# Kernel tuning notes

Hardware: AMD Instinct MI355X
Metric: run time of the kernel (lower is better)

## Reference

```python
import jax, jax.numpy as jnp
import numpy as np

LEAKING_RATE = 0.5

def setup_inputs() -> dict:
    key = jax.random.key(0)
    k1, k2, k3 = jax.random.split(key, 3)
    B, T, I, R = 32, 4096, 64, 512
    x = jax.random.normal(k1, (B, T, I), dtype=jnp.float32)
    # input_projection weight ~ U(-1, 1), shape [R, I]
    w_in = jax.random.uniform(k2, (R, I), dtype=jnp.float32, minval=-1.0, maxval=1.0)
    # state_projection diagonal ~ U(-0.5, 0.5)
    d = jax.random.uniform(k3, (R,), dtype=jnp.float32, minval=-0.5, maxval=0.5)
    return {"x": x, "w_in": w_in, "d": d}

def reference(x, w_in, d):
    # Faithful to the original forward: the Python loop reads all_states[:, t, :],
    # which is ZERO at every step (never the previous state). Hence each timestep
    # is independent:
    #   state = 0
    #   new_state = tanh(d * state + x_t @ W_in^T) = tanh(x_t @ W_in^T)
    #   out_t = lr * state + (1 - lr) * new_state = (1 - lr) * tanh(x_t @ W_in^T)
    proj = jnp.einsum('bti,ri->btr', x, w_in)           # [B, T, R]
    zero_state = jnp.zeros_like(proj)
    new_state = jnp.tanh(zero_state * d + proj)
    out = LEAKING_RATE * zero_state + (1.0 - LEAKING_RATE) * new_state
    return out
```

## Files before the change

kernel.cpp:

```cpp
#include <hip/hip_runtime.h>

typedef int   i32x4 __attribute__((ext_vector_type(4)));
typedef float f32x4 __attribute__((ext_vector_type(4)));

#define M_ROWS 131072
#define N_COLS 512
#define K_DIM  64
#define MT     4
#define MAGIC  0x600DF00D

#define MFMAI8 __builtin_amdgcn_mfma_i32_16x16x64_i8

__device__ __forceinline__ int obuf_idx(int m, int r) {
  return m * 512 + (r ^ ((m & 7) << 2));
}

__device__ __forceinline__ void lds_barrier() {
  asm volatile("s_waitcnt lgkmcnt(0)" ::: "memory");
  __builtin_amdgcn_s_barrier();
  __builtin_amdgcn_sched_barrier(0);
}

__device__ __forceinline__ float half_tanh_pre(float ps) {
  float t = __builtin_amdgcn_exp2f(ps);
  return 0.5f - __builtin_amdgcn_rcpf(t + 1.0f);
}

__device__ __forceinline__ void xquant16(const float* __restrict__ p,
                                         i32x4& hi, i32x4& lo) {
#pragma unroll
  for (int c = 0; c < 4; ++c) {
    f32x4 v = *(const f32x4*)(p + 4 * c);
    int a1 = 0, a0 = 0;
#pragma unroll
    for (int j = 0; j < 4; ++j) {
      float s = __builtin_rintf(v[j] * 2048.0f);
      s = fminf(fmaxf(s, -16319.f), 16319.f);
      const int q = (int)s;
      const int h = (q + 64) >> 7;
      const int l = q - (h << 7);
      a1 |= (h & 255) << (8 * j);
      a0 |= (l & 255) << (8 * j);
    }
    hi[c] = a1; lo[c] = a0;
  }
}

__global__ void probe_k(int* __restrict__ tab,
                        i32x4* __restrict__ wq1, i32x4* __restrict__ wq0,
                        const float* __restrict__ w) {
  const int tid  = threadIdx.x;
  const int lane = tid & 63;
  const int i16  = lane & 15;
  const int g    = lane >> 4;
  const i32x4 zi = {0, 0, 0, 0};

  int pig[4];
  bool ok = true;
  {
    const int bb = (g + 1) * 0x01010101;
    const i32x4 bgv = {bb, bb, bb, bb};
#pragma unroll
    for (int g0 = 0; g0 < 4; ++g0) {
      const int ab = (g == g0) ? 0x01010101 : 0;
      const i32x4 dA = {ab, ab, ab, ab};
      i32x4 dt = MFMAI8(dA, bgv, zi, 0, 0, 0);
      const int v = dt[0] >> 4;
      bool u = (dt[0] == (v << 4)) && (v >= 1) && (v <= 4);
#pragma unroll
      for (int q = 1; q < 4; ++q) u = u && (dt[q] == dt[0]);
      ok = ok && u;
      pig[g0] = v - 1;
    }
  }
  ok = ok && (((1 << pig[0]) | (1 << pig[1]) | (1 << pig[2]) | (1 << pig[3])) == 15);
  int pinv_g = 0;
#pragma unroll
  for (int g0 = 0; g0 < 4; ++g0) if (pig[g0] == g) pinv_g = g0;

  int rowv[4], colv[4];
  {
    const int vb = i16 * 0x01010101;
    const i32x4 vals  = {vb, vb, vb, vb};
    const i32x4 onesv = {0x01010101, 0x01010101, 0x01010101, 0x01010101};
    i32x4 d1 = MFMAI8(vals, onesv, zi, 0, 0, 0);
    i32x4 d2 = MFMAI8(onesv, vals, zi, 0, 0, 0);
#pragma unroll
    for (int q = 0; q < 4; ++q) {
      rowv[q] = d1[q] >> 6;
      colv[q] = d2[q] >> 6;
      ok = ok && (d1[q] == (rowv[q] << 6)) && (rowv[q] >= 0) && (rowv[q] < 16) &&
                 (d2[q] == (colv[q] << 6)) && (colv[q] >= 0) && (colv[q] < 16);
    }
  }

  {
    i32x4 ta, tb;
#pragma unroll
    for (int c = 0; c < 4; ++c) {
      int a = 0, b = 0;
#pragma unroll
      for (int j = 0; j < 4; ++j) {
        const int ka = 16 * g + 4 * c + j;
        const int kb = 16 * pinv_g + 4 * c + j;
        const int av = ((5 * i16 + 3 * ka) & 63) - 32;
        const int bv = ((7 * kb + 11 * i16) & 63) - 32;
        a |= (av & 255) << (8 * j);
        b |= (bv & 255) << (8 * j);
      }
      ta[c] = a; tb[c] = b;
    }
    i32x4 dt3 = MFMAI8(ta, tb, zi, 0, 0, 0);
#pragma unroll
    for (int q = 0; q < 4; ++q) {
      int ref = 0;
      for (int k = 0; k < 64; ++k)
        ref += (((5 * rowv[q] + 3 * k) & 63) - 32) * (((7 * k + 11 * colv[q]) & 63) - 32);
      ok = ok && (dt3[q] == ref);
    }
  }
  const bool all_ok = __all((int)ok);
  const bool vec = all_ok &&
      __all((int)(colv[0] == colv[1] && colv[1] == colv[2] && colv[2] == colv[3] &&
                  rowv[1] == rowv[0] + 1 && rowv[2] == rowv[0] + 2 &&
                  rowv[3] == rowv[0] + 3 && (rowv[0] & 3) == 0));

  if (tid < 64) {
#pragma unroll
    for (int q = 0; q < 4; ++q) tab[lane * 4 + q] = (colv[q] << 8) | rowv[q];
    tab[256 + lane] = pinv_g;
    if (lane == 0) { tab[320] = all_ok ? MAGIC : 0; tab[321] = vec ? 1 : 0; }
  }

  if (wq1 != nullptr) {
    const float* wr = w + (size_t)tid * K_DIM;
#pragma unroll
    for (int gg = 0; gg < 4; ++gg) {
      i32x4 a1v, a0v;
#pragma unroll
      for (int c = 0; c < 4; ++c) {
        int a1 = 0, a0 = 0;
#pragma unroll
        for (int j = 0; j < 4; ++j) {
          float s = __builtin_rintf(wr[16 * gg + 4 * c + j] * 8192.0f);
          s = fminf(fmaxf(s, -8192.f), 8192.f);
          const int q = (int)s;
          const int h = (q + 64) >> 7;
          const int l = q - (h << 7);
          a1 |= (h & 255) << (8 * j);
          a0 |= (l & 255) << (8 * j);
        }
        a1v[c] = a1; a0v[c] = a0;
      }
      wq1[tid * 4 + gg] = a1v;
      wq0[tid * 4 + gg] = a0v;
    }
  }
}

__global__ __launch_bounds__(256, 4) void esn_m(const float* __restrict__ x,
                                                const float* __restrict__ w,
                                                const int* __restrict__ tab,
                                                const i32x4* __restrict__ wq1,
                                                const i32x4* __restrict__ wq0,
                                                float* __restrict__ out) {
  const int tid  = threadIdx.x;
  const int wv   = tid >> 6;
  const int lane = tid & 63;
  const int i16  = lane & 15;
  const int g    = lane >> 4;
  const int mb0  = blockIdx.x * (16 * MT);
  const i32x4 zi = {0, 0, 0, 0};

  __shared__ int   xq[MT][2][64][4];
  __shared__ float obuf[16 * 512];

  bool ok = false;
  int vecf = 0, pinv = 0;
  int rowv[4], colv[4];
  if (tab != nullptr) {
    const i32x4 rc = ((const i32x4*)tab)[lane];
#pragma unroll
    for (int q = 0; q < 4; ++q) { rowv[q] = rc[q] & 255; colv[q] = (rc[q] >> 8) & 255; }
    pinv = tab[256 + lane];
    ok   = (tab[320] == MAGIC);
    vecf = tab[321];
  }

  if (ok) {
    {
      i32x4 x1p, x0p;
      xquant16(x + (size_t)(mb0 + 16 * wv + i16) * K_DIM + 16 * pinv, x1p, x0p);
      *(i32x4*)&xq[wv][0][lane][0] = x1p;
      *(i32x4*)&xq[wv][1][lane][0] = x0p;
    }

    i32x4 w1p[8], w0p[8];
    if (wq1 != nullptr) {
#pragma unroll
      for (int t = 0; t < 8; ++t) {
        const int row = 128 * wv + 16 * t + i16;
        w1p[t] = wq1[row * 4 + g];
        w0p[t] = wq0[row * 4 + g];
      }
    } else {
#pragma unroll
      for (int t = 0; t < 8; ++t) {
        const float* wb = w + (size_t)(128 * wv + 16 * t + i16) * K_DIM + 16 * g;
#pragma unroll
        for (int c = 0; c < 4; ++c) {
          f32x4 v = *(const f32x4*)(wb + 4 * c);
          int a1 = 0, a0 = 0;
#pragma unroll
          for (int j = 0; j < 4; ++j) {
            float s = __builtin_rintf(v[j] * 8192.0f);
            s = fminf(fmaxf(s, -8192.f), 8192.f);
            const int q = (int)s;
            const int h = (q + 64) >> 7;
            const int l = q - (h << 7);
            a1 |= (h & 255) << (8 * j);
            a0 |= (l & 255) << (8 * j);
          }
          w1p[t][c] = a1; w0p[t][c] = a0;
        }
      }
    }
    __syncthreads();

    const float TANH_C = 2.8853900817779268f * 5.9604644775390625e-8f;
#pragma unroll 1
    for (int mi = 0; mi < MT; ++mi) {
      const int mb = mb0 + 16 * mi;
      const i32x4 x1p = *(const i32x4*)&xq[mi][0][lane][0];
      const i32x4 x0p = *(const i32x4*)&xq[mi][1][lane][0];

#pragma unroll
      for (int t = 0; t < 8; ++t) {
        i32x4 p11 = MFMAI8(w1p[t], x1p, zi, 0, 0, 0);
        i32x4 pm  = MFMAI8(w0p[t], x1p, zi, 0, 0, 0);
        pm        = MFMAI8(w1p[t], x0p, pm, 0, 0, 0);
        i32x4 p00 = MFMAI8(w0p[t], x0p, zi, 0, 0, 0);

        const int rb = 128 * wv + 16 * t;
        if (vecf) {
          f32x4 v;
#pragma unroll
          for (int q = 0; q < 4; ++q) {
            const float S = fmaf((float)p11[q], 16384.f,
                                 fmaf((float)pm[q], 128.f, (float)p00[q]));
            v[q] = half_tanh_pre(S * TANH_C);
          }
          *(f32x4*)&obuf[obuf_idx(colv[0], rb + rowv[0])] = v;
        } else {
#pragma unroll
          for (int q = 0; q < 4; ++q) {
            const float S = fmaf((float)p11[q], 16384.f,
                                 fmaf((float)pm[q], 128.f, (float)p00[q]));
            obuf[obuf_idx(colv[q], rb + rowv[q])] = half_tanh_pre(S * TANH_C);
          }
        }
      }
      lds_barrier();

#pragma unroll
      for (int p = 0; p < 8; ++p) {
        const int idx = p * 1024 + tid * 4;
        const int row = idx >> 9, col = idx & 511;
        const f32x4 v = *(const f32x4*)&obuf[obuf_idx(row, col)];
        *(f32x4*)(out + (size_t)mb * N_COLS + idx) = v;
      }
      if (mi + 1 < MT) lds_barrier();
    }
  } else {
#pragma unroll 1
    for (int half = 0; half < 2; ++half) {
      const int r = half * 256 + tid;
      f32x4 wr[16];
      const f32x4* wp = (const f32x4*)(w + (size_t)r * K_DIM);
#pragma unroll
      for (int i = 0; i < 16; ++i) wr[i] = wp[i];

      const f32x4* xrow = (const f32x4*)(x + (size_t)mb0 * K_DIM);
      float* orow = out + (size_t)mb0 * N_COLS + r;
#pragma unroll 1
      for (int mi = 0; mi < 16 * MT; ++mi) {
        const f32x4* xr = xrow + (size_t)mi * 16;
        f32x4 acc = {0.f, 0.f, 0.f, 0.f};
#pragma unroll
        for (int kc = 0; kc < 16; kc += 4)
#pragma unroll
          for (int j = 0; j < 4; ++j) {
            acc[0] = fmaf(xr[kc + 0][j], wr[kc + 0][j], acc[0]);
            acc[1] = fmaf(xr[kc + 1][j], wr[kc + 1][j], acc[1]);
            acc[2] = fmaf(xr[kc + 2][j], wr[kc + 2][j], acc[2]);
            acc[3] = fmaf(xr[kc + 3][j], wr[kc + 3][j], acc[3]);
          }
        const float p = (acc[0] + acc[1]) + (acc[2] + acc[3]);
        orow[(size_t)mi * N_COLS] = half_tanh_pre(p * 2.8853900817779268f);
      }
    }
  }
}

extern "C" void kernel_launch(void* const* d_in, const int* in_sizes, int n_in,
                              void* d_out, int out_size, void* d_ws, size_t ws_size,
                              hipStream_t stream) {
  const float* x = (const float*)d_in[0];
  const float* w = (const float*)d_in[1];
  float* out = (float*)d_out;

  int*   tab = (ws_size >= 2048) ? (int*)d_ws : nullptr;
  i32x4* wq1 = nullptr;
  i32x4* wq0 = nullptr;
  if (ws_size >= 4096 + 2 * 32768) {
    wq1 = (i32x4*)((char*)d_ws + 4096);
    wq0 = (i32x4*)((char*)d_ws + 4096 + 32768);
  }
  if (tab) hipLaunchKernelGGL(probe_k, dim3(1), dim3(512), 0, stream,
                              tab, wq1, wq0, w);

  dim3 grid(M_ROWS / (16 * MT));
  dim3 block(256);
  hipLaunchKernelGGL(esn_m, grid, block, 0, stream, x, w, tab, wq1, wq0, out);
}
```

Measured before the change: 83.41 us.

## Split block into producer and consumer warps with double-buffered LDS flags

Replaces the barrier-synchronised compute-then-store loop with warp specialisation. Four producer waves run the int8 MFMA work and tanh into a double-buffered LDS tile, and four consumer waves copy finished tiles to global memory, coordinated by spin-waited LDS flags. The block grows to 512 threads with 8 row tiles per block, and x is quantised into registers instead of LDS. This aims to overlap compute with output stores and drop full-block barriers. In exchange it lowers occupancy to one block per CU, halves the grid, and adds spin-wait overhead.

```diff
diff --git a/kernel.cpp b/kernel.cpp
--- a/kernel.cpp
+++ b/kernel.cpp
@@ -6,19 +6,13 @@
 #define M_ROWS 131072
 #define N_COLS 512
 #define K_DIM  64
-#define MT     4
+#define MT     8
 #define MAGIC  0x600DF00D
 
 #define MFMAI8 __builtin_amdgcn_mfma_i32_16x16x64_i8
 
 __device__ __forceinline__ int obuf_idx(int m, int r) {
   return m * 512 + (r ^ ((m & 7) << 2));
-}
-
-__device__ __forceinline__ void lds_barrier() {
-  asm volatile("s_waitcnt lgkmcnt(0)" ::: "memory");
-  __builtin_amdgcn_s_barrier();
-  __builtin_amdgcn_sched_barrier(0);
 }
 
 __device__ __forceinline__ float half_tanh_pre(float ps) {
@@ -46,6 +40,10 @@
   }
 }
 
+__device__ __forceinline__ void spin_until_ge(volatile int* f, int v) {
+  while (*f < v) asm volatile("s_sleep 1");
+}
+
 __global__ void probe_k(int* __restrict__ tab,
                         i32x4* __restrict__ wq1, i32x4* __restrict__ wq0,
                         const float* __restrict__ w) {
@@ -158,12 +156,12 @@
   }
 }
 
-__global__ __launch_bounds__(256, 4) void esn_m(const float* __restrict__ x,
-                                                const float* __restrict__ w,
-                                                const int* __restrict__ tab,
-                                                const i32x4* __restrict__ wq1,
-                                                const i32x4* __restrict__ wq0,
-                                                float* __restrict__ out) {
+__global__ __launch_bounds__(512, 1) void esn_pc(const float* __restrict__ x,
+                                                 const float* __restrict__ w,
+                                                 const int* __restrict__ tab,
+                                                 const i32x4* __restrict__ wq1,
+                                                 const i32x4* __restrict__ wq0,
+                                                 float* __restrict__ out) {
   const int tid  = threadIdx.x;
   const int wv   = tid >> 6;
   const int lane = tid & 63;
@@ -172,8 +170,9 @@
   const int mb0  = blockIdx.x * (16 * MT);
   const i32x4 zi = {0, 0, 0, 0};
 
-  __shared__ int   xq[MT][2][64][4];
-  __shared__ float obuf[16 * 512];
+  __shared__ float obuf[2][16 * 512];
+  volatile __shared__ int pf[2][4];
+  volatile __shared__ int cf[2][4];
 
   bool ok = false;
   int vecf = 0, pinv = 0;
@@ -187,117 +186,134 @@
     vecf = tab[321];
   }
 
+  if (tid < 4) { pf[0][tid] = 0; pf[1][tid] = 0; cf[0][tid] = 0; cf[1][tid] = 0; }
+  __syncthreads();
+
   if (ok) {
-    {
-      i32x4 x1p, x0p;
-      xquant16(x + (size_t)(mb0 + 16 * wv + i16) * K_DIM + 16 * pinv, x1p, x0p);
-      *(i32x4*)&xq[wv][0][lane][0] = x1p;
-      *(i32x4*)&xq[wv][1][lane][0] = x0p;
-    }
-
-    i32x4 w1p[8], w0p[8];
-    if (wq1 != nullptr) {
-#pragma unroll
-      for (int t = 0; t < 8; ++t) {
-        const int row = 128 * wv + 16 * t + i16;
-        w1p[t] = wq1[row * 4 + g];
-        w0p[t] = wq0[row * 4 + g];
+    if (wv < 4) {
+      const int pw = wv;
+
+      i32x4 xt1[MT], xt0[MT];
+#pragma unroll
+      for (int mi = 0; mi < MT; ++mi)
+        xquant16(x + (size_t)(mb0 + 16 * mi + i16) * K_DIM + 16 * pinv,
+                 xt1[mi], xt0[mi]);
+
+      i32x4 w1p[8], w0p[8];
+      if (wq1 != nullptr) {
+#pragma unroll
+        for (int t = 0; t < 8; ++t) {
+          const int row = 128 * pw + 16 * t + i16;
+          w1p[t] = wq1[row * 4 + g];
+          w0p[t] = wq0[row * 4 + g];
+        }
+      } else {
+#pragma unroll
+        for (int t = 0; t < 8; ++t) {
+          const float* wb = w + (size_t)(128 * pw + 16 * t + i16) * K_DIM + 16 * g;
+#pragma unroll
+          for (int c = 0; c < 4; ++c) {
+            f32x4 v = *(const f32x4*)(wb + 4 * c);
+            int a1 = 0, a0 = 0;
+#pragma unroll
+            for (int j = 0; j < 4; ++j) {
+              float s = __builtin_rintf(v[j] * 8192.0f);
+              s = fminf(fmaxf(s, -8192.f), 8192.f);
+              const int q = (int)s;
+              const int h = (q + 64) >> 7;
+              const int l = q - (h << 7);
+              a1 |= (h & 255) << (8 * j);
+              a0 |= (l & 255) << (8 * j);
+            }
+            w1p[t][c] = a1; w0p[t][c] = a0;
+          }
+        }
+      }
+
+      const float TANH_C = 2.8853900817779268f * 5.9604644775390625e-8f;
+#pragma unroll
+      for (int mi = 0; mi < MT; ++mi) {
+        const int b = mi & 1, gen = mi >> 1;
+#pragma unroll
+        for (int cw = 0; cw < 4; ++cw) spin_until_ge(&cf[b][cw], gen);
+        __builtin_amdgcn_sched_barrier(0);
+
+        float* buf = obuf[b];
+#pragma unroll
+        for (int t = 0; t < 8; ++t) {
+          i32x4 p11 = MFMAI8(w1p[t], xt1[mi], zi, 0, 0, 0);
+          i32x4 pm  = MFMAI8(w0p[t], xt1[mi], zi, 0, 0, 0);
+          pm        = MFMAI8(w1p[t], xt0[mi], pm, 0, 0, 0);
+          i32x4 p00 = MFMAI8(w0p[t], xt0[mi], zi, 0, 0, 0);
+
+          const int rb = 128 * pw + 16 * t;
+          if (vecf) {
+            f32x4 v;
+#pragma unroll
+            for (int q = 0; q < 4; ++q) {
+              const float S = fmaf((float)p11[q], 16384.f,
+                                   fmaf((float)pm[q], 128.f, (float)p00[q]));
+              v[q] = half_tanh_pre(S * TANH_C);
+            }
+            *(f32x4*)&buf[obuf_idx(colv[0], rb + rowv[0])] = v;
+          } else {
+#pragma unroll
+            for (int q = 0; q < 4; ++q) {
+              const float S = fmaf((float)p11[q], 16384.f,
+                                   fmaf((float)pm[q], 128.f, (float)p00[q]));
+              buf[obuf_idx(colv[q], rb + rowv[q])] = half_tanh_pre(S * TANH_C);
+            }
+          }
+        }
+        asm volatile("s_waitcnt lgkmcnt(0)" ::: "memory");
+        pf[b][pw] = gen + 1;
       }
     } else {
-#pragma unroll
-      for (int t = 0; t < 8; ++t) {
-        const float* wb = w + (size_t)(128 * wv + 16 * t + i16) * K_DIM + 16 * g;
-#pragma unroll
-        for (int c = 0; c < 4; ++c) {
-          f32x4 v = *(const f32x4*)(wb + 4 * c);
-          int a1 = 0, a0 = 0;
-#pragma unroll
-          for (int j = 0; j < 4; ++j) {
-            float s = __builtin_rintf(v[j] * 8192.0f);
-            s = fminf(fmaxf(s, -8192.f), 8192.f);
-            const int q = (int)s;
-            const int h = (q + 64) >> 7;
-            const int l = q - (h << 7);
-            a1 |= (h & 255) << (8 * j);
-            a0 |= (l & 255) << (8 * j);
-          }
-          w1p[t][c] = a1; w0p[t][c] = a0;
-        }
-      }
-    }
-    __syncthreads();
-
-    const float TANH_C = 2.8853900817779268f * 5.9604644775390625e-8f;
+      const int cw = wv - 4;
 #pragma unroll 1
-    for (int mi = 0; mi < MT; ++mi) {
-      const int mb = mb0 + 16 * mi;
-      const i32x4 x1p = *(const i32x4*)&xq[mi][0][lane][0];
-      const i32x4 x0p = *(const i32x4*)&xq[mi][1][lane][0];
-
-#pragma unroll
-      for (int t = 0; t < 8; ++t) {
-        i32x4 p11 = MFMAI8(w1p[t], x1p, zi, 0, 0, 0);
-        i32x4 pm  = MFMAI8(w0p[t], x1p, zi, 0, 0, 0);
-        pm        = MFMAI8(w1p[t], x0p, pm, 0, 0, 0);
-        i32x4 p00 = MFMAI8(w0p[t], x0p, zi, 0, 0, 0);
-
-        const int rb = 128 * wv + 16 * t;
-        if (vecf) {
-          f32x4 v;
-#pragma unroll
-          for (int q = 0; q < 4; ++q) {
-            const float S = fmaf((float)p11[q], 16384.f,
-                                 fmaf((float)pm[q], 128.f, (float)p00[q]));
-            v[q] = half_tanh_pre(S * TANH_C);
-          }
-          *(f32x4*)&obuf[obuf_idx(colv[0], rb + rowv[0])] = v;
-        } else {
-#pragma unroll
-          for (int q = 0; q < 4; ++q) {
-            const float S = fmaf((float)p11[q], 16384.f,
-                                 fmaf((float)pm[q], 128.f, (float)p00[q]));
-            obuf[obuf_idx(colv[q], rb + rowv[q])] = half_tanh_pre(S * TANH_C);
-          }
-        }
-      }
-      lds_barrier();
-
-#pragma unroll
-      for (int p = 0; p < 8; ++p) {
-        const int idx = p * 1024 + tid * 4;
-        const int row = idx >> 9, col = idx & 511;
-        const f32x4 v = *(const f32x4*)&obuf[obuf_idx(row, col)];
-        *(f32x4*)(out + (size_t)mb * N_COLS + idx) = v;
-      }
-      if (mi + 1 < MT) lds_barrier();
+      for (int mi = 0; mi < MT; ++mi) {
+        const int b = mi & 1, gen = mi >> 1;
+#pragma unroll
+        for (int pw = 0; pw < 4; ++pw) spin_until_ge(&pf[b][pw], gen + 1);
+        __builtin_amdgcn_sched_barrier(0);
+
+        const float* buf = obuf[b];
+        float* dst = out + (size_t)(mb0 + 16 * mi) * N_COLS;
+#pragma unroll
+        for (int j = 0; j < 8; ++j) {
+          const int f = cw * 2048 + j * 256 + lane * 4;
+          const int m = f >> 9, r = f & 511;
+          const f32x4 v = *(const f32x4*)&buf[obuf_idx(m, r)];
+          *(f32x4*)(dst + f) = v;
+        }
+        asm volatile("s_waitcnt lgkmcnt(0)" ::: "memory");
+        cf[b][cw] = gen + 1;
+      }
     }
   } else {
+    const int r = tid;
+    f32x4 wr[16];
+    const f32x4* wp = (const f32x4*)(w + (size_t)r * K_DIM);
+#pragma unroll
+    for (int i = 0; i < 16; ++i) wr[i] = wp[i];
+
+    const f32x4* xrow = (const f32x4*)(x + (size_t)mb0 * K_DIM);
+    float* orow = out + (size_t)mb0 * N_COLS + r;
 #pragma unroll 1
-    for (int half = 0; half < 2; ++half) {
-      const int r = half * 256 + tid;
-      f32x4 wr[16];
-      const f32x4* wp = (const f32x4*)(w + (size_t)r * K_DIM);
-#pragma unroll
-      for (int i = 0; i < 16; ++i) wr[i] = wp[i];
-
-      const f32x4* xrow = (const f32x4*)(x + (size_t)mb0 * K_DIM);
-      float* orow = out + (size_t)mb0 * N_COLS + r;
-#pragma unroll 1
-      for (int mi = 0; mi < 16 * MT; ++mi) {
-        const f32x4* xr = xrow + (size_t)mi * 16;
-        f32x4 acc = {0.f, 0.f, 0.f, 0.f};
-#pragma unroll
-        for (int kc = 0; kc < 16; kc += 4)
-#pragma unroll
-          for (int j = 0; j < 4; ++j) {
-            acc[0] = fmaf(xr[kc + 0][j], wr[kc + 0][j], acc[0]);
-            acc[1] = fmaf(xr[kc + 1][j], wr[kc + 1][j], acc[1]);
-            acc[2] = fmaf(xr[kc + 2][j], wr[kc + 2][j], acc[2]);
-            acc[3] = fmaf(xr[kc + 3][j], wr[kc + 3][j], acc[3]);
-          }
-        const float p = (acc[0] + acc[1]) + (acc[2] + acc[3]);
-        orow[(size_t)mi * N_COLS] = half_tanh_pre(p * 2.8853900817779268f);
-      }
+    for (int mi = 0; mi < 16 * MT; ++mi) {
+      const f32x4* xr = xrow + (size_t)mi * 16;
+      f32x4 acc = {0.f, 0.f, 0.f, 0.f};
+#pragma unroll
+      for (int kc = 0; kc < 16; kc += 4)
+#pragma unroll
+        for (int j = 0; j < 4; ++j) {
+          acc[0] = fmaf(xr[kc + 0][j], wr[kc + 0][j], acc[0]);
+          acc[1] = fmaf(xr[kc + 1][j], wr[kc + 1][j], acc[1]);
+          acc[2] = fmaf(xr[kc + 2][j], wr[kc + 2][j], acc[2]);
+          acc[3] = fmaf(xr[kc + 3][j], wr[kc + 3][j], acc[3]);
+        }
+      const float p = (acc[0] + acc[1]) + (acc[2] + acc[3]);
+      orow[(size_t)mi * N_COLS] = half_tanh_pre(p * 2.8853900817779268f);
     }
   }
 }
@@ -320,6 +336,6 @@
                               tab, wq1, wq0, w);
 
   dim3 grid(M_ROWS / (16 * MT));
-  dim3 block(256);
-  hipLaunchKernelGGL(esn_m, grid, block, 0, stream, x, w, tab, wq1, wq0, out);
-}
+  dim3 block(512);
+  hipLaunchKernelGGL(esn_pc, grid, block, 0, stream, x, w, tab, wq1, wq0, out);
+}
```

Result: slower. 108.3 us (+29.8%).
